# Kernel optimization log

Measured on AMD Instinct MI355X. Metric: run time of the kernel, lower is better.

## Reference

```python
import jax, jax.numpy as jnp
import numpy as np

D = 2524
EXP = 4
EPS = 1e-8

def _rmsnorm(x, scale):
    # p=-1 default: full RMSNorm, rms = ||x||_2 / sqrt(d)
    rms = jnp.sqrt(jnp.sum(x * x, axis=-1, keepdims=True)) * (D ** -0.5)
    return scale * (x / (rms + EPS))

def setup_inputs() -> dict:
    key = jax.random.key(0)
    ks = jax.random.split(key, 16)
    S, B = 512, 32
    H = EXP * D
    s = 0.02
    return {
        'x': jax.random.normal(ks[0], (S, B, D), jnp.float32),
        'y': jax.random.normal(ks[1], (S, B), jnp.float32),
        'mask': jnp.ones((B, S), jnp.float32),
        'norm1_scale': jnp.ones((D,), jnp.float32),
        'norm2_scale': jnp.ones((D,), jnp.float32),
        'w1': jax.random.normal(ks[2], (H, D), jnp.float32) * s,
        'b1': jnp.zeros((H,), jnp.float32),
        'w2': jax.random.normal(ks[3], (D, H), jnp.float32) * s,
        'b2': jnp.zeros((D,), jnp.float32),
        'att_w': jax.random.normal(ks[4], (D, D), jnp.float32) * s,
        'att_b': jnp.zeros((D,), jnp.float32),
        'lin_w': jax.random.normal(ks[5], (D, D), jnp.float32) * s,
        'lin_b': jnp.zeros((D,), jnp.float32),
        'fc_w': jax.random.normal(ks[6], (6, D), jnp.float32) * s,
        'fc_b': jnp.zeros((6,), jnp.float32),
    }

def reference(x, y, mask, norm1_scale, norm2_scale, w1, b1, w2, b2,
              att_w, att_b, lin_w, lin_b, fc_w, fc_b):
    # x: (S, B, D); mask: (B, S)
    residual = x
    x = jnp.fft.fft2(x, axes=(-1, -2)).real                 # FNet token/feature mixing
    x = _rmsnorm(x + residual, norm1_scale)
    residual = x
    h = jax.nn.gelu(x @ w1.T + b1, approximate=False)       # (S,B,4D), dropout=identity (eval)
    x = h @ w2.T + b2
    emotions = _rmsnorm(x + residual, norm2_scale)           # (S,B,D)

    # MatchingAttention 'general2', vectorized over all query positions t
    q = emotions @ att_w.T + att_b                           # (S,B,D)
    Mm = emotions * mask.T[:, :, None]                       # mask memory: (S,B,D)
    scores = jnp.einsum('tbd,sbd->bts', q, Mm) * mask[:, None, :]
    a = jax.nn.softmax(jnp.tanh(scores), axis=-1)
    a = a * mask[:, None, :]
    a = a / jnp.sum(a, axis=-1, keepdims=True)               # (B,T,S)
    att_emotions = jnp.einsum('bts,sbd->tbd', a, emotions)   # (S,B,D)
    alpha = jnp.transpose(a, (1, 0, 2))                      # (T,B,S): stacked alpha_[:,0,:]

    hidden = jax.nn.relu(att_emotions @ lin_w.T + lin_b)     # (S,B,D)
    log_prob = hidden @ fc_w.T + fc_b                        # (S,B,6)
    return (log_prob, alpha)
```

## Files before the change

### kernel.cpp

```cpp
#include <hip/hip_runtime.h>
#include <hip/hip_bf16.h>
#include <math.h>

#define SLEN 512
#define BATCH 32
#define DIM 2524
#define DK 2560
#define NTOK 16384
#define LD1 2560
#define LDH 5120

using f32x4 = __attribute__((ext_vector_type(4))) float;
using bfrag = __attribute__((ext_vector_type(8))) short;

__device__ __forceinline__ short f2bs(float f) {
  __hip_bfloat16 h = __float2bfloat16(f);
  return *reinterpret_cast<short*>(&h);
}
__device__ __forceinline__ float bs2f(short s) {
  __hip_bfloat16 h;
  *reinterpret_cast<short*>(&h) = s;
  return __bfloat162float(h);
}

__device__ __forceinline__ void gload16(const short* g, short* l) {
  __builtin_amdgcn_global_load_lds(
      (const __attribute__((address_space(1))) void*)g,
      (__attribute__((address_space(3))) void*)l, 16, 0, 0);
}

__global__ void k_conv_pad(const float* __restrict__ in, short* __restrict__ out,
                           int Min, int Kin, int Mout, int Kout, int roff, int coff) {
  const int cpr = Kout >> 2;
  long idx = (long)blockIdx.x * 256 + threadIdx.x;
  if (idx >= (long)Mout * cpr) return;
  int r = (int)(idx / cpr);
  int c4 = (int)(idx % cpr) * 4;
  short4 o;
#pragma unroll
  for (int j = 0; j < 4; j++) {
    int c = c4 + j;
    float v = (roff + r < Min && coff + c < Kin) ? in[(long)(roff + r) * Kin + coff + c] : 0.f;
    ((short*)&o)[j] = f2bs(v);
  }
  *(short4*)(out + (long)r * Kout + c4) = o;
}

__global__ void k_gen_cs2(short* __restrict__ out) {
  const int cpr = LDH >> 2;
  long idx = (long)blockIdx.x * 256 + threadIdx.x;
  if (idx >= (long)LD1 * cpr) return;
  int r = (int)(idx / cpr);
  int c4 = (int)(idx % cpr) * 4;
  short4 o;
#pragma unroll
  for (int j = 0; j < 4; j++) {
    int c = c4 + j;
    float v = 0.f;
    if (r < DIM) {
      if (c < DIM) {
        int mm = (c * r) % DIM;
        v = cosf((float)mm * (6.2831853071795864f / (float)DIM));
      } else if (c >= LD1 && c < LD1 + DIM) {
        int mm = ((c - LD1) * r) % DIM;
        v = -sinf((float)mm * (6.2831853071795864f / (float)DIM));
      }
    }
    ((short*)&o)[j] = f2bs(v);
  }
  *(short4*)(out + (long)r * LDH + c4) = o;
}

__global__ __launch_bounds__(256) void k_bmix1(const float* __restrict__ x,
                                               short* __restrict__ xri) {
  __shared__ float xs[32][64];
  __shared__ float tc[32][32];
  __shared__ float ts[32][32];
  const int s = blockIdx.x;
  const int d0 = blockIdx.y * 64;
  const int tid = threadIdx.x;
  for (int j = tid; j < 1024; j += 256) {
    int bp = j >> 5, b = j & 31;
    float th = (float)((b * bp) & 31) * (6.2831853071795864f / 32.f);
    tc[bp][b] = cosf(th);
    ts[bp][b] = sinf(th);
  }
#pragma unroll
  for (int j = 0; j < 8; j++) {
    int lin = j * 256 + tid;
    int b = lin >> 6, dd = lin & 63;
    int d = d0 + dd;
    xs[b][dd] = (d < DIM) ? x[((long)s * 32 + b) * DIM + d] : 0.f;
  }
  __syncthreads();
  const int g = tid >> 6, dd = tid & 63;
  const int d = d0 + dd;
  const bool ok = d < DIM;
#pragma unroll
  for (int j = 0; j < 8; j++) {
    int bp = g * 8 + j;
    float P = 0.f, Q = 0.f;
#pragma unroll
    for (int b = 0; b < 32; b++) {
      float v = xs[b][dd];
      P += v * tc[bp][b];
      Q += v * ts[bp][b];
    }
    long row = (long)s * 32 + bp;
    xri[row * LDH + d] = ok ? f2bs(P) : (short)0;
    xri[row * LDH + LD1 + d] = ok ? f2bs(Q) : (short)0;
  }
}

__global__ __launch_bounds__(512, 2) void gemm256(
    const short* __restrict__ A, long lda,
    const short* __restrict__ Bt, long ldb,
    void* __restrict__ Cout, long ldc,
    int N, int nzero, int K,
    const float* __restrict__ bias,
    const float* __restrict__ res, long ldres,
    int gn, int epi) {
  __shared__ __align__(16) short lds[65536];
  const int tid = threadIdx.x;
  const int w = tid >> 6;
  const int l = tid & 63;
  const int nwg = gridDim.x;
  const int lin = blockIdx.x;
  const int swz = (lin & 7) * (nwg >> 3) + (lin >> 3);
  const int bm = swz / gn, bn = swz % gn;
  const long row0 = (long)bm * 256;
  const long col0 = (long)bn * 256;
  const int wm = w >> 2, wn = w & 3;
  const short* Ab = A + row0 * lda;
  const short* Bb = Bt + col0 * ldb;
  const int rloc = l & 15;
  const int kslot = l >> 4;

  f32x4 acc[8][4] = {};
  bfrag af[4], bf[4];
  const int nt = K >> 6;

#define STAGEA(bufbit, ks, L, kt)                                              \
  {                                                                            \
    const short* gsrc = Ab + (long)(((L) * 8 + w) * 16 + rloc) * lda +         \
                        (long)(kt) * 64 + (ks) * 32 + kslot * 8;               \
    short* ldst = &lds[(bufbit) * 32768 + (ks) * 8192 + ((L) * 8 + w) * 512];  \
    gload16(gsrc, ldst);                                                       \
  }
#define STAGEB(bufbit, ks, L, kt)                                              \
  {                                                                            \
    const short* gsrc = Bb + (long)(((L) * 8 + w) * 16 + rloc) * ldb +         \
                        (long)(kt) * 64 + (ks) * 32 + kslot * 8;               \
    short* ldst = &lds[(bufbit) * 32768 + 16384 + (ks) * 8192 + ((L) * 8 + w) * 512]; \
    gload16(gsrc, ldst);                                                       \
  }
#define LDAF(buf, i, ks) \
  (*(const bfrag*)&lds[(buf) * 32768 + (ks) * 8192 + (wm * 8 + (i)) * 512 + kslot * 128 + rloc * 8])
#define LDBF(buf, j, ks) \
  (*(const bfrag*)&lds[(buf) * 32768 + 16384 + (ks) * 8192 + (wn * 4 + (j)) * 512 + kslot * 128 + rloc * 8])

  STAGEA(0, 0, 0, 0) STAGEA(0, 0, 1, 0)
  STAGEB(0, 0, 0, 0) STAGEB(0, 0, 1, 0)
  STAGEA(0, 1, 0, 0) STAGEA(0, 1, 1, 0)
  STAGEB(0, 1, 0, 0) STAGEB(0, 1, 1, 0)
  asm volatile("s_waitcnt vmcnt(4)" ::: "memory");
  __builtin_amdgcn_s_barrier();

  for (int t = 0; t < nt; ++t) {
    const int cur = t & 1, nb = cur ^ 1;
    const int ktn = (t + 1 < nt) ? t + 1 : t;
#pragma unroll
    for (int i = 0; i < 4; i++) af[i] = LDAF(cur, i, 0);
#pragma unroll
    for (int j = 0; j < 4; j++) bf[j] = LDBF(cur, j, 0);
    STAGEA(nb, 0, 0, ktn) STAGEA(nb, 0, 1, ktn)
    __builtin_amdgcn_s_barrier();
    asm volatile("s_waitcnt lgkmcnt(0)" ::: "memory");
    __builtin_amdgcn_sched_barrier(0);
    __builtin_amdgcn_s_setprio(1);
#pragma unroll
    for (int i = 0; i < 4; i++)
#pragma unroll
      for (int j = 0; j < 4; j++)
        acc[i][j] = __builtin_amdgcn_mfma_f32_16x16x32_bf16(af[i], bf[j], acc[i][j], 0, 0, 0);
    __builtin_amdgcn_s_setprio(0);
    __builtin_amdgcn_s_barrier();
#pragma unroll
    for (int i = 0; i < 4; i++) af[i] = LDAF(cur, 4 + i, 0);
    STAGEB(nb, 0, 0, ktn) STAGEB(nb, 0, 1, ktn)
    __builtin_amdgcn_s_barrier();
    asm volatile("s_waitcnt lgkmcnt(0)" ::: "memory");
    __builtin_amdgcn_sched_barrier(0);
    __builtin_amdgcn_s_setprio(1);
#pragma unroll
    for (int i = 0; i < 4; i++)
#pragma unroll
      for (int j = 0; j < 4; j++)
        acc[4 + i][j] = __builtin_amdgcn_mfma_f32_16x16x32_bf16(af[i], bf[j], acc[4 + i][j], 0, 0, 0);
    __builtin_amdgcn_s_setprio(0);
    asm volatile("s_waitcnt vmcnt(4)" ::: "memory");
    __builtin_amdgcn_s_barrier();
#pragma unroll
    for (int i = 0; i < 4; i++) af[i] = LDAF(cur, i, 1);
#pragma unroll
    for (int j = 0; j < 4; j++) bf[j] = LDBF(cur, j, 1);
    STAGEA(nb, 1, 0, ktn) STAGEA(nb, 1, 1, ktn)
    __builtin_amdgcn_s_barrier();
    asm volatile("s_waitcnt lgkmcnt(0)" ::: "memory");
    __builtin_amdgcn_sched_barrier(0);
    __builtin_amdgcn_s_setprio(1);
#pragma unroll
    for (int i = 0; i < 4; i++)
#pragma unroll
      for (int j = 0; j < 4; j++)
        acc[i][j] = __builtin_amdgcn_mfma_f32_16x16x32_bf16(af[i], bf[j], acc[i][j], 0, 0, 0);
    __builtin_amdgcn_s_setprio(0);
    __builtin_amdgcn_s_barrier();
#pragma unroll
    for (int i = 0; i < 4; i++) af[i] = LDAF(cur, 4 + i, 1);
    STAGEB(nb, 1, 0, ktn) STAGEB(nb, 1, 1, ktn)
    __builtin_amdgcn_s_barrier();
    asm volatile("s_waitcnt lgkmcnt(0)" ::: "memory");
    __builtin_amdgcn_sched_barrier(0);
    __builtin_amdgcn_s_setprio(1);
#pragma unroll
    for (int i = 0; i < 4; i++)
#pragma unroll
      for (int j = 0; j < 4; j++)
        acc[4 + i][j] = __builtin_amdgcn_mfma_f32_16x16x32_bf16(af[i], bf[j], acc[4 + i][j], 0, 0, 0);
    __builtin_amdgcn_s_setprio(0);
    asm volatile("s_waitcnt vmcnt(4)" ::: "memory");
    __builtin_amdgcn_s_barrier();
  }
  asm volatile("s_waitcnt vmcnt(0)" ::: "memory");

  float* outF = (float*)Cout;
  __hip_bfloat16* outB = (__hip_bfloat16*)Cout;
  const int erow = kslot * 4;
  const int ecol = rloc;
#pragma unroll
  for (int i = 0; i < 8; i++) {
#pragma unroll
    for (int e = 0; e < 4; e++) {
      long grow = row0 + wm * 128 + i * 16 + erow + e;
#pragma unroll
      for (int j = 0; j < 4; j++) {
        int gcol = (int)col0 + wn * 64 + j * 16 + ecol;
        if (gcol >= nzero) continue;
        float v = 0.f;
        if (gcol < N) {
          v = acc[i][j][e];
          if (bias) v += bias[gcol];
          if (epi == 1) v += res[grow * ldres + gcol];
          else if (epi == 2) v = 0.5f * v * (1.f + erff(v * 0.70710678118f));
          else if (epi == 4) v = fmaxf(v, 0.f);
        }
        if (epi == 6) outF[grow * ldc + gcol] += v;
        else if (epi <= 1) outF[grow * ldc + gcol] = v;
        else outB[grow * ldc + gcol] = __float2bfloat16(v);
      }
    }
  }
#undef STAGEA
#undef STAGEB
#undef LDAF
#undef LDBF
}

__global__ __launch_bounds__(256) void gemm_bt(
    const short* __restrict__ A, long sA, long lda,
    const short* __restrict__ Bt, long sB, long ldb,
    void* __restrict__ Cout, long sC, long ldc,
    int N, int nzero, int K,
    const float* __restrict__ bias,
    const float* __restrict__ mask, long sMask,
    int epi) {
  __shared__ __align__(16) short As[4096];
  __shared__ __align__(16) short Bs[4096];
  const int tid = threadIdx.x;
  const int wave = tid >> 6;
  const int lane = tid & 63;
  const int z = blockIdx.z;
  const long row0 = (long)blockIdx.x * 128;
  const long col0 = (long)blockIdx.y * 128;
  const int wm = wave >> 1, wn = wave & 1;
  const short* Ab = A + z * sA + row0 * lda;
  const short* Bb = Bt + z * sB + col0 * ldb;
  const int r0 = tid >> 2, c0 = (tid & 3) * 8;
  const int r1 = r0 + 64;
  short* dA0 = As + (wave << 9);
  short* dA1 = As + 2048 + (wave << 9);
  short* dB0 = Bs + (wave << 9);
  short* dB1 = Bs + 2048 + (wave << 9);
  f32x4 acc[4][4] = {};
  for (int k0 = 0; k0 < K; k0 += 32) {
    __syncthreads();
    gload16(Ab + (long)r0 * lda + k0 + c0, dA0);
    gload16(Ab + (long)r1 * lda + k0 + c0, dA1);
    gload16(Bb + (long)r0 * ldb + k0 + c0, dB0);
    gload16(Bb + (long)r1 * ldb + k0 + c0, dB1);
    __syncthreads();
    const int kb = (lane >> 4) << 3;
    const int rr = lane & 15;
    bfrag a[4], b[4];
#pragma unroll
    for (int i = 0; i < 4; i++)
      a[i] = *(const bfrag*)&As[(wm * 64 + i * 16 + rr) * 32 + kb];
#pragma unroll
    for (int j = 0; j < 4; j++)
      b[j] = *(const bfrag*)&Bs[(wn * 64 + j * 16 + rr) * 32 + kb];
#pragma unroll
    for (int i = 0; i < 4; i++)
#pragma unroll
      for (int j = 0; j < 4; j++)
        acc[i][j] = __builtin_amdgcn_mfma_f32_16x16x32_bf16(a[i], b[j], acc[i][j], 0, 0, 0);
  }
  float* outF = (float*)Cout + z * sC;
  __hip_bfloat16* outB = (__hip_bfloat16*)Cout + z * sC;
  const float* mz = mask ? mask + z * sMask : nullptr;
  const int erow = (lane >> 4) * 4;
  const int ecol = lane & 15;
#pragma unroll
  for (int i = 0; i < 4; i++) {
#pragma unroll
    for (int e = 0; e < 4; e++) {
      long grow = row0 + wm * 64 + i * 16 + erow + e;
#pragma unroll
      for (int j = 0; j < 4; j++) {
        int gcol = (int)col0 + wn * 64 + j * 16 + ecol;
        if (gcol >= nzero) continue;
        float v = 0.f;
        if (gcol < N) {
          v = acc[i][j][e];
          if (bias) v += bias[gcol];
          if (epi == 5) v = tanhf(v * mz[gcol]);
        }
        if (epi == 5) outF[grow * ldc + gcol] = v;
        else outB[grow * ldc + gcol] = __float2bfloat16(v);
      }
    }
  }
}

__global__ __launch_bounds__(256) void k_rms(const float* __restrict__ in, long ldin,
                                             const float* __restrict__ scale,
                                             float* __restrict__ outf,
                                             short* __restrict__ outb1,
                                             short* __restrict__ outb2,
                                             const float* __restrict__ mask) {
  const long row = blockIdx.x;
  const float* rp = in + row * ldin;
  const int tid = threadIdx.x;
  float ss = 0.f;
  for (int d = tid; d < DIM; d += 256) { float v = rp[d]; ss = fmaf(v, v, ss); }
  __shared__ float red[4];
  for (int o = 32; o; o >>= 1) ss += __shfl_down(ss, o);
  if ((tid & 63) == 0) red[tid >> 6] = ss;
  __syncthreads();
  float tot = red[0] + red[1] + red[2] + red[3];
  float rms = sqrtf(tot * (1.f / (float)DIM));
  float inv = 1.f / (rms + 1e-8f);
  float mf = 1.f;
  if (mask) mf = mask[(row & 31) * SLEN + (int)(row >> 5)];
  for (int d = tid; d < DK; d += 256) {
    float v = (d < DIM) ? rp[d] * inv * scale[d] : 0.f;
    if (outf) outf[row * DK + d] = v;
    if (outb1) outb1[row * DK + d] = f2bs(v);
    if (outb2) outb2[row * DK + d] = f2bs(v * mf);
  }
}

__global__ __launch_bounds__(256) void k_transpose(const short* __restrict__ emob,
                                                   short* __restrict__ emoT) {
  __shared__ short t[64][66];
  const int b = blockIdx.z;
  const int d0 = blockIdx.y * 64;
  const int s0 = blockIdx.x * 64;
  const int tid = threadIdx.x;
#pragma unroll
  for (int j = 0; j < 16; j++) {
    int lin = j * 256 + tid;
    int r = lin >> 6, c = lin & 63;
    int d = d0 + c;
    t[r][c] = (d < DIM) ? emob[((long)(s0 + r) * 32 + b) * DK + d] : (short)0;
  }
  __syncthreads();
#pragma unroll
  for (int j = 0; j < 16; j++) {
    int lin = j * 256 + tid;
    int r = lin >> 6, c = lin & 63;
    emoT[((long)b * 2560 + d0 + r) * SLEN + s0 + c] = t[c][r];
  }
}

__global__ __launch_bounds__(256) void k_softmax(const float* __restrict__ sc,
                                                 const float* __restrict__ mask,
                                                 float* __restrict__ alpha,
                                                 short* __restrict__ ab) {
  const int r = blockIdx.x;
  const int b = r >> 9, tq = r & 511;
  const float* row = sc + (long)r * SLEN;
  const int tid = threadIdx.x;
  const int lane = tid & 63, wv = tid >> 6;
  __shared__ float red[4];
  float v0 = row[tid], v1 = row[tid + 256];
  float m = fmaxf(v0, v1);
  for (int o = 32; o; o >>= 1) m = fmaxf(m, __shfl_down(m, o));
  if (lane == 0) red[wv] = m;
  __syncthreads();
  m = fmaxf(fmaxf(red[0], red[1]), fmaxf(red[2], red[3]));
  __syncthreads();
  float e0 = expf(v0 - m), e1 = expf(v1 - m);
  float s = e0 + e1;
  for (int o = 32; o; o >>= 1) s += __shfl_down(s, o);
  if (lane == 0) red[wv] = s;
  __syncthreads();
  s = red[0] + red[1] + red[2] + red[3];
  __syncthreads();
  float m0 = mask[b * SLEN + tid], m1 = mask[b * SLEN + tid + 256];
  float a0 = e0 / s * m0, a1 = e1 / s * m1;
  float s2 = a0 + a1;
  for (int o = 32; o; o >>= 1) s2 += __shfl_down(s2, o);
  if (lane == 0) red[wv] = s2;
  __syncthreads();
  s2 = red[0] + red[1] + red[2] + red[3];
  float f0 = a0 / s2, f1 = a1 / s2;
  long ob = ((long)tq * BATCH + b) * SLEN;
  alpha[ob + tid] = f0;
  alpha[ob + tid + 256] = f1;
  ab[(long)r * SLEN + tid] = f2bs(f0);
  ab[(long)r * SLEN + tid + 256] = f2bs(f1);
}

__global__ __launch_bounds__(256) void k_logprob(const short* __restrict__ hid,
                                                 const float* __restrict__ fcw,
                                                 const float* __restrict__ fcb,
                                                 float* __restrict__ out) {
  const int tok = blockIdx.x * 4 + (threadIdx.x >> 6);
  const int lane = threadIdx.x & 63;
  const short* hr = hid + (long)tok * DK;
  float p0 = 0, p1 = 0, p2 = 0, p3 = 0, p4 = 0, p5 = 0;
  for (int d = lane; d < DIM; d += 64) {
    float h = bs2f(hr[d]);
    p0 += h * fcw[d];
    p1 += h * fcw[DIM + d];
    p2 += h * fcw[2 * DIM + d];
    p3 += h * fcw[3 * DIM + d];
    p4 += h * fcw[4 * DIM + d];
    p5 += h * fcw[5 * DIM + d];
  }
  for (int o = 32; o; o >>= 1) {
    p0 += __shfl_down(p0, o); p1 += __shfl_down(p1, o); p2 += __shfl_down(p2, o);
    p3 += __shfl_down(p3, o); p4 += __shfl_down(p4, o); p5 += __shfl_down(p5, o);
  }
  if (lane == 0) {
    float* o6 = out + (long)tok * 6;
    o6[0] = p0 + fcb[0]; o6[1] = p1 + fcb[1]; o6[2] = p2 + fcb[2];
    o6[3] = p3 + fcb[3]; o6[4] = p4 + fcb[4]; o6[5] = p5 + fcb[5];
  }
}

extern "C" void kernel_launch(void* const* d_in, const int* in_sizes, int n_in,
                              void* d_out, int out_size, void* d_ws, size_t ws_size,
                              hipStream_t stream) {
  const float* x    = (const float*)d_in[0];
  const float* mask = (const float*)d_in[2];
  const float* n1s  = (const float*)d_in[3];
  const float* n2s  = (const float*)d_in[4];
  const float* w1   = (const float*)d_in[5];
  const float* b1   = (const float*)d_in[6];
  const float* w2   = (const float*)d_in[7];
  const float* b2   = (const float*)d_in[8];
  const float* attw = (const float*)d_in[9];
  const float* att_bias = (const float*)d_in[10];
  const float* linw = (const float*)d_in[11];
  const float* lin_bias = (const float*)d_in[12];
  const float* fcw  = (const float*)d_in[13];
  const float* fcb  = (const float*)d_in[14];
  float* out = (float*)d_out;

  const size_t R2 = 0;
  const size_t R3 = 167772160;
  const size_t R4 = 335544320;
  const size_t RF = 419430400;
  const size_t TOTAL = 445644800;
  if (ws_size < TOTAL) return;

  char* ws = (char*)d_ws;
  float* t1   = (float*)(ws + R2);
  short* hbH  = (short*)(ws + R2);
  short* emob = (short*)(ws + R2);
  short* mmb  = (short*)(ws + R2 + 83886080);
  float* scr  = (float*)(ws + R2);
  short* ab   = (short*)(ws + R2 + 33554432);
  short* xri  = (short*)(ws + R3);
  float* x1f  = (float*)(ws + R3);
  float* t2   = x1f;
  short* atb  = (short*)(ws + R3);
  short* emoT = (short*)(ws + R3 + 83886080);
  short* x1b  = (short*)(ws + R4);
  short* qb   = (short*)(ws + R4);
  short* hidb = (short*)(ws + R4);
  short* wtb  = (short*)(ws + RF);

  dim3 blk(256), blk5(512);
  k_bmix1<<<dim3(512, 40), blk, 0, stream>>>(x, xri);
  k_gen_cs2<<<dim3((LD1 * (LDH / 4) + 255) / 256), blk, 0, stream>>>(wtb);
  gemm256<<<dim3(640), blk5, 0, stream>>>(xri, LDH, wtb, LDH, t1, LD1,
                                          DIM, 2560, LDH, nullptr, x, DIM, 10, 1);
  k_rms<<<dim3(NTOK), blk, 0, stream>>>(t1, LD1, n1s, x1f, x1b, nullptr, nullptr);
  k_conv_pad<<<dim3((5120 * 640 + 255) / 256), blk, 0, stream>>>(w1, wtb, 10096, 2524, 5120, 2560, 0, 0);
  gemm256<<<dim3(1280), blk5, 0, stream>>>(x1b, DK, wtb, DK, hbH, LDH,
                                           5120, 5120, DK, b1, nullptr, 0, 20, 2);
  k_conv_pad<<<dim3((2560 * 1280 + 255) / 256), blk, 0, stream>>>(w2, wtb, 2524, 10096, 2560, 5120, 0, 0);
  gemm256<<<dim3(640), blk5, 0, stream>>>(hbH, LDH, wtb, LDH, t2, DK,
                                          DIM, 2560, LDH, b2, x1f, DK, 10, 1);
  k_conv_pad<<<dim3((5120 * 640 + 255) / 256), blk, 0, stream>>>(w1, wtb, 10096, 2524, 5120, 2560, 5120, 0);
  gemm256<<<dim3(1280), blk5, 0, stream>>>(x1b, DK, wtb, DK, hbH, LDH,
                                           4976, 5120, DK, b1 + 5120, nullptr, 0, 20, 2);
  k_conv_pad<<<dim3((2560 * 1280 + 255) / 256), blk, 0, stream>>>(w2, wtb, 2524, 10096, 2560, 5120, 0, 5120);
  gemm256<<<dim3(640), blk5, 0, stream>>>(hbH, LDH, wtb, LDH, t2, DK,
                                          2560, 2560, LDH, nullptr, nullptr, 0, 10, 6);
  k_rms<<<dim3(NTOK), blk, 0, stream>>>(t2, DK, n2s, nullptr, emob, mmb, mask);
  k_transpose<<<dim3(8, 40, 32), blk, 0, stream>>>(emob, emoT);
  k_conv_pad<<<dim3((2560 * 640 + 255) / 256), blk, 0, stream>>>(attw, wtb, 2524, 2524, 2560, 2560, 0, 0);
  gemm256<<<dim3(640), blk5, 0, stream>>>(emob, DK, wtb, DK, qb, DK,
                                          DIM, 2560, DK, att_bias, nullptr, 0, 10, 3);
  gemm_bt<<<dim3(4, 4, 32), blk, 0, stream>>>(qb, DK, (long)BATCH * DK, mmb, DK, (long)BATCH * DK,
                                              scr, (long)SLEN * SLEN, SLEN,
                                              SLEN, SLEN, DK, nullptr, mask, SLEN, 5);
  k_softmax<<<dim3(NTOK), blk, 0, stream>>>(scr, mask, out + 98304, ab);
  gemm_bt<<<dim3(4, 20, 32), blk, 0, stream>>>(ab, (long)SLEN * SLEN, SLEN, emoT, (long)2560 * SLEN, SLEN,
                                               atb, DK, (long)BATCH * DK,
                                               2560, 2560, SLEN, nullptr, nullptr, 0, 3);
  k_conv_pad<<<dim3((2560 * 640 + 255) / 256), blk, 0, stream>>>(linw, wtb, 2524, 2524, 2560, 2560, 0, 0);
  gemm256<<<dim3(640), blk5, 0, stream>>>(atb, DK, wtb, DK, hidb, DK,
                                          DIM, 2560, DK, lin_bias, nullptr, 0, 10, 4);
  k_logprob<<<dim3(NTOK / 4), blk, 0, stream>>>(hidb, fcw, fcb, out);
}
```

Before: 5.037 ms.

## Reorder FNet 2D DFT: real-input half-spectrum GEMM on features, then batch mix

The 2D DFT real part is restructured. Previously the small batch-axis DFT ran first and produced complex bf16 data, followed by a K=5120 GEMM against a combined cos/sin matrix. Now the feature-axis DFT runs first as a K=2560 GEMM whose output holds only the non-redundant half-spectrum (cos and -sin rows, using Hermitian symmetry). A batch-mix kernel then rebuilds the full spectrum and adds the residual in fp32. This halves the GEMM's K dimension and removes the wide complex intermediate, at the cost of an extra bf16 conversion of x and an fp32 intermediate. The GEMM tile swizzle is also changed to group tiles into 16x2 blocks for better L2 reuse, which assumes grid and gn divisibility.

New measurement: 5.030 ms. No clear change (-0.1%).

```diff
diff --git a/kernel.cpp b/kernel.cpp
--- a/kernel.cpp
+++ b/kernel.cpp
@@ -9,6 +9,7 @@
 #define NTOK 16384
 #define LD1 2560
 #define LDH 5120
+#define DHALF 1280
 
 using f32x4 = __attribute__((ext_vector_type(4))) float;
 using bfrag = __attribute__((ext_vector_type(8))) short;
@@ -46,34 +47,33 @@
   *(short4*)(out + (long)r * Kout + c4) = o;
 }
 
-__global__ void k_gen_cs2(short* __restrict__ out) {
-  const int cpr = LDH >> 2;
+__global__ void k_gen_csD(short* __restrict__ out) {
+  const int cpr = DK >> 2;
   long idx = (long)blockIdx.x * 256 + threadIdx.x;
-  if (idx >= (long)LD1 * cpr) return;
+  if (idx >= (long)DK * cpr) return;
   int r = (int)(idx / cpr);
   int c4 = (int)(idx % cpr) * 4;
+  const int dp = (r < DHALF) ? r : r - DHALF;
   short4 o;
 #pragma unroll
   for (int j = 0; j < 4; j++) {
     int c = c4 + j;
     float v = 0.f;
-    if (r < DIM) {
-      if (c < DIM) {
-        int mm = (c * r) % DIM;
-        v = cosf((float)mm * (6.2831853071795864f / (float)DIM));
-      } else if (c >= LD1 && c < LD1 + DIM) {
-        int mm = ((c - LD1) * r) % DIM;
-        v = -sinf((float)mm * (6.2831853071795864f / (float)DIM));
-      }
+    if (dp <= 1262 && c < DIM) {
+      int mm = (c * dp) % DIM;
+      float th = (float)mm * (6.2831853071795864f / (float)DIM);
+      v = (r < DHALF) ? cosf(th) : -sinf(th);
     }
     ((short*)&o)[j] = f2bs(v);
   }
-  *(short4*)(out + (long)r * LDH + c4) = o;
-}
-
-__global__ __launch_bounds__(256) void k_bmix1(const float* __restrict__ x,
-                                               short* __restrict__ xri) {
-  __shared__ float xs[32][64];
+  *(short4*)(out + (long)r * DK + c4) = o;
+}
+
+__global__ __launch_bounds__(256) void k_bmix2(const float* __restrict__ yri,
+                                               const float* __restrict__ x,
+                                               float* __restrict__ t1) {
+  __shared__ float yr[32][64];
+  __shared__ float yi[32][64];
   __shared__ float tc[32][32];
   __shared__ float ts[32][32];
   const int s = blockIdx.x;
@@ -90,25 +90,34 @@
     int lin = j * 256 + tid;
     int b = lin >> 6, dd = lin & 63;
     int d = d0 + dd;
-    xs[b][dd] = (d < DIM) ? x[((long)s * 32 + b) * DIM + d] : 0.f;
+    float vr = 0.f, vi = 0.f;
+    if (d < DIM) {
+      const float* rowp = yri + ((long)s * 32 + b) * DK;
+      if (d <= 1262) {
+        vr = rowp[d];
+        vi = rowp[DHALF + d];
+      } else {
+        int dm = DIM - d;
+        vr = rowp[dm];
+        vi = -rowp[DHALF + dm];
+      }
+    }
+    yr[b][dd] = vr;
+    yi[b][dd] = vi;
   }
   __syncthreads();
   const int g = tid >> 6, dd = tid & 63;
   const int d = d0 + dd;
-  const bool ok = d < DIM;
+  if (d >= DIM) return;
 #pragma unroll
   for (int j = 0; j < 8; j++) {
     int bp = g * 8 + j;
-    float P = 0.f, Q = 0.f;
-#pragma unroll
-    for (int b = 0; b < 32; b++) {
-      float v = xs[b][dd];
-      P += v * tc[bp][b];
-      Q += v * ts[bp][b];
-    }
+    float acc = 0.f;
+#pragma unroll
+    for (int b = 0; b < 32; b++)
+      acc += yr[b][dd] * tc[bp][b] + yi[b][dd] * ts[bp][b];
     long row = (long)s * 32 + bp;
-    xri[row * LDH + d] = ok ? f2bs(P) : (short)0;
-    xri[row * LDH + LD1 + d] = ok ? f2bs(Q) : (short)0;
+    t1[row * DK + d] = acc + x[row * DIM + d];
   }
 }
 
@@ -125,9 +134,12 @@
   const int w = tid >> 6;
   const int l = tid & 63;
   const int nwg = gridDim.x;
-  const int lin = blockIdx.x;
-  const int swz = (lin & 7) * (nwg >> 3) + (lin >> 3);
-  const int bm = swz / gn, bn = swz % gn;
+  const int cpx = nwg >> 3;
+  const int g = (blockIdx.x & 7) * cpx + (blockIdx.x >> 3);
+  const int C = g >> 5, r32 = g & 31;
+  const int nbn = gn >> 1;
+  const int bm = (C / nbn) * 16 + (r32 >> 1);
+  const int bn = (C % nbn) * 2 + (r32 & 1);
   const long row0 = (long)bm * 256;
   const long col0 = (long)bn * 256;
   const int wm = w >> 2, wn = w & 3;
@@ -487,27 +499,29 @@
   if (ws_size < TOTAL) return;
 
   char* ws = (char*)d_ws;
-  float* t1   = (float*)(ws + R2);
+  float* yri  = (float*)(ws + R2);
   short* hbH  = (short*)(ws + R2);
   short* emob = (short*)(ws + R2);
   short* mmb  = (short*)(ws + R2 + 83886080);
   float* scr  = (float*)(ws + R2);
   short* ab   = (short*)(ws + R2 + 33554432);
-  short* xri  = (short*)(ws + R3);
-  float* x1f  = (float*)(ws + R3);
-  float* t2   = x1f;
+  float* t1   = (float*)(ws + R3);
+  float* x1f  = t1;
+  float* t2   = t1;
   short* atb  = (short*)(ws + R3);
   short* emoT = (short*)(ws + R3 + 83886080);
+  short* xb   = (short*)(ws + R4);
   short* x1b  = (short*)(ws + R4);
   short* qb   = (short*)(ws + R4);
   short* hidb = (short*)(ws + R4);
   short* wtb  = (short*)(ws + RF);
 
   dim3 blk(256), blk5(512);
-  k_bmix1<<<dim3(512, 40), blk, 0, stream>>>(x, xri);
-  k_gen_cs2<<<dim3((LD1 * (LDH / 4) + 255) / 256), blk, 0, stream>>>(wtb);
-  gemm256<<<dim3(640), blk5, 0, stream>>>(xri, LDH, wtb, LDH, t1, LD1,
-                                          DIM, 2560, LDH, nullptr, x, DIM, 10, 1);
+  k_conv_pad<<<dim3((16384 * 640 + 255) / 256), blk, 0, stream>>>(x, xb, 16384, 2524, 16384, 2560, 0, 0);
+  k_gen_csD<<<dim3((2560 * 640 + 255) / 256), blk, 0, stream>>>(wtb);
+  gemm256<<<dim3(640), blk5, 0, stream>>>(xb, 2560, wtb, 2560, yri, 2560,
+                                          2560, 2560, 2560, nullptr, nullptr, 0, 10, 0);
+  k_bmix2<<<dim3(512, 40), blk, 0, stream>>>(yri, x, t1);
   k_rms<<<dim3(NTOK), blk, 0, stream>>>(t1, LD1, n1s, x1f, x1b, nullptr, nullptr);
   k_conv_pad<<<dim3((5120 * 640 + 255) / 256), blk, 0, stream>>>(w1, wtb, 10096, 2524, 5120, 2560, 0, 0);
   gemm256<<<dim3(1280), blk5, 0, stream>>>(x1b, DK, wtb, DK, hbH, LDH,
```
